# Performance work log

Hardware: AMD Instinct MI355X
Metric: run time of the kernel (lower is better)

## Reference

```python
import jax, jax.numpy as jnp
import numpy as np

B, S, HID = 2, 2048, 2048
NH, NKV, D = 32, 8, 64
G = NH // NKV
THETA = 150000.0


def rotate_half(x):
    x1, x2 = x[..., : D // 2], x[..., D // 2 :]
    return jnp.concatenate([-x2, x1], axis=-1)


def setup_inputs() -> dict:
    key = jax.random.key(0)
    ks = jax.random.split(key, 10)
    sc = 0.02
    return {
        "hidden_states": jax.random.normal(ks[0], (B, S, HID), jnp.float32),
        "position_ids": jnp.arange(S, dtype=jnp.int64 if jax.config.jax_enable_x64 else jnp.int32),
        "wq": jax.random.normal(ks[1], (HID, NH * D), jnp.float32) * sc,
        "bq": jax.random.normal(ks[2], (NH * D,), jnp.float32) * sc,
        "wk": jax.random.normal(ks[3], (HID, NKV * D), jnp.float32) * sc,
        "bk": jax.random.normal(ks[4], (NKV * D,), jnp.float32) * sc,
        "wv": jax.random.normal(ks[5], (HID, NKV * D), jnp.float32) * sc,
        "bv": jax.random.normal(ks[6], (NKV * D,), jnp.float32) * sc,
        "wo": jax.random.normal(ks[7], (NH * D, HID), jnp.float32) * sc,
        "bo": jax.random.normal(ks[8], (HID,), jnp.float32) * sc,
    }


def reference(hidden_states, position_ids, wq, bq, wk, bk, wv, bv, wo, bo):
    # projections: [B,S,NH,D] / [B,S,NKV,D] -> head-major
    q = (hidden_states @ wq + bq).reshape(B, S, NH, D).transpose(0, 2, 1, 3)   # [B,NH,S,D]
    k = (hidden_states @ wk + bk).reshape(B, S, NKV, D).transpose(0, 2, 1, 3)  # [B,NKV,S,D]
    v = (hidden_states @ wv + bv).reshape(B, S, NKV, D).transpose(0, 2, 1, 3)

    # HF RoPE: inv_freq over even dims, freqs duplicated across the two halves
    inv_freq = 1.0 / (THETA ** (jnp.arange(0, D, 2, dtype=jnp.float32) / D))   # [D/2]
    freqs = position_ids.astype(jnp.float32)[:, None] * inv_freq[None, :]      # [S,D/2]
    emb = jnp.concatenate([freqs, freqs], axis=-1)                             # [S,D]
    cos = jnp.cos(emb)[None, None]  # [1,1,S,D]
    sin = jnp.sin(emb)[None, None]
    q = q * cos + rotate_half(q) * sin
    k = k * cos + rotate_half(k) * sin

    # GQA: group query heads by kv head instead of repeat_interleave on K/V
    qg = q.reshape(B, NKV, G, S, D)
    scores = jnp.einsum("bkgsd,bktd->bkgst", qg, k) / jnp.sqrt(jnp.float32(D))  # [B,NKV,G,S,S]
    attn = jax.nn.softmax(scores, axis=-1)
    out = jnp.einsum("bkgst,bktd->bkgsd", attn, v)                              # [B,NKV,G,S,D]
    out = out.reshape(B, NH, S, D).transpose(0, 2, 1, 3).reshape(B, S, NH * D)  # [B,S,NH*D]
    return out @ wo + bo
```

## Files before the change

### kernel.cpp

```cpp
#include <hip/hip_runtime.h>
#include <hip/hip_bf16.h>
#include <math.h>

#define B_   2
#define S_   2048
#define HID_ 2048
#define NH_  32
#define NKV_ 8
#define D_   64
#define G_   (NH_/NKV_)
#define M_   (B_*S_)

typedef __hip_bfloat16 bf16;
typedef short bf16x8 __attribute__((ext_vector_type(8)));
typedef float f32x4  __attribute__((ext_vector_type(4)));
typedef unsigned short u16x4 __attribute__((ext_vector_type(4)));

__device__ inline unsigned short f2bfu(float f){
    __hip_bfloat16 h = __float2bfloat16(f);
    return __builtin_bit_cast(unsigned short, h);
}

__device__ __forceinline__ float fexp2(float x){
#if __has_builtin(__builtin_amdgcn_exp2f)
    return __builtin_amdgcn_exp2f(x);
#else
    return exp2f(x);
#endif
}

__device__ __forceinline__ void async16(const void* g, void* l) {
    __builtin_amdgcn_global_load_lds(
        (const __attribute__((address_space(1))) unsigned int*)g,
        (__attribute__((address_space(3))) unsigned int*)l, 16, 0, 0);
}

__global__ __launch_bounds__(256) void cvt_k(
    const float* __restrict__ src, bf16* __restrict__ dst, int n)
{
    const int i = (blockIdx.x * 256 + threadIdx.x) * 8;
    if (i >= n) return;
    const float4 a = *(const float4*)(src + i);
    const float4 b = *(const float4*)(src + i + 4);
    uint4 u;
    u.x = (unsigned)f2bfu(a.x) | ((unsigned)f2bfu(a.y) << 16);
    u.y = (unsigned)f2bfu(a.z) | ((unsigned)f2bfu(a.w) << 16);
    u.z = (unsigned)f2bfu(b.x) | ((unsigned)f2bfu(b.y) << 16);
    u.w = (unsigned)f2bfu(b.z) | ((unsigned)f2bfu(b.w) << 16);
    *(uint4*)((unsigned short*)dst + i) = u;
}

__global__ __launch_bounds__(256) void wtrans_k(
    const float* __restrict__ s0, int N0,
    const float* __restrict__ s1, int N1,
    const float* __restrict__ s2, int N2,
    bf16* __restrict__ dst, int K)
{
    __shared__ unsigned short t[64][65];
    const int ntile = blockIdx.x * 64, ktile = blockIdx.y * 64;
    const float* src; int nloc, Nseg;
    if (ntile < N0)           { src = s0; nloc = ntile;           Nseg = N0; }
    else if (ntile < N0 + N1) { src = s1; nloc = ntile - N0;      Nseg = N1; }
    else                      { src = s2; nloc = ntile - N0 - N1; Nseg = N2; }
    const int r  = threadIdx.x >> 4;
    const int c4 = (threadIdx.x & 15) * 4;
    #pragma unroll
    for (int p = 0; p < 4; p++) {
        const int k = p * 16 + r;
        const float4 f = *(const float4*)(src + (size_t)(ktile + k) * Nseg + nloc + c4);
        t[k][c4+0] = f2bfu(f.x); t[k][c4+1] = f2bfu(f.y);
        t[k][c4+2] = f2bfu(f.z); t[k][c4+3] = f2bfu(f.w);
    }
    __syncthreads();
    #pragma unroll
    for (int p = 0; p < 4; p++) {
        const int n = p * 16 + r;
        u16x4 u = { t[c4+0][n], t[c4+1][n], t[c4+2][n], t[c4+3][n] };
        *(u16x4*)((unsigned short*)dst + (size_t)(ntile + n) * K + ktile + c4) = u;
    }
}

__global__ __launch_bounds__(256) void rope_tab_k(
    const int* __restrict__ pos, float* __restrict__ ctab, float* __restrict__ stab)
{
    const int idx = blockIdx.x * 256 + threadIdx.x;
    if (idx >= S_ * 32) return;
    const int s = idx >> 5, i = idx & 31;
    const int is64 = (pos[1] == 0);
    const int p = is64 ? pos[2 * s] : pos[s];
    const double inv = exp(-(double)i * (log(150000.0) / 32.0));
    const double f = (double)p * inv;
    ctab[idx] = (float)cos(f);
    stab[idx] = (float)sin(f);
}

template<int MODE>
__global__ __launch_bounds__(256) void gemm128_k(
    const bf16* __restrict__ A, const bf16* __restrict__ WT,
    const float* __restrict__ b0, const float* __restrict__ b1,
    const float* __restrict__ b2,
    bf16* __restrict__ Cq, bf16* __restrict__ Ck, bf16* __restrict__ Cv,
    float* __restrict__ Cout,
    const float* __restrict__ ctab, const float* __restrict__ stab)
{
    __shared__ unsigned short sA[128 * 64];
    __shared__ unsigned short sB[128 * 64];

    const int tid  = threadIdx.x;
    const int wave = tid >> 6, lane = tid & 63;
    const int li   = lane & 15, lj = lane >> 4;
    const int m0   = blockIdx.y * 128;
    const int n0   = blockIdx.x * 128;
    const int wm   = (wave >> 1) * 64, wn = (wave & 1) * 64;
    const int K    = 2048;

    f32x4 acc[4][4];
    #pragma unroll
    for (int i = 0; i < 4; i++)
        #pragma unroll
        for (int j = 0; j < 4; j++)
            acc[i][j] = (f32x4){0.f, 0.f, 0.f, 0.f};

    const bf16* ag = A  + (size_t)(m0 + wave * 32 + (lane >> 3)) * K + (lane & 7) * 8;
    const bf16* bg = WT + (size_t)(n0 + wave * 32 + (lane >> 3)) * K + (lane & 7) * 8;
    unsigned short* la = &sA[(wave * 32) * 64];
    unsigned short* lb = &sB[(wave * 32) * 64];

    for (int k0 = 0; k0 < K; k0 += 64) {
        __syncthreads();
        #pragma unroll
        for (int i = 0; i < 4; i++) {
            async16(ag + k0 + (size_t)i * 8 * K, la + i * 8 * 64);
            async16(bg + k0 + (size_t)i * 8 * K, lb + i * 8 * 64);
        }
        __syncthreads();

        #pragma unroll
        for (int ks = 0; ks < 64; ks += 32) {
            bf16x8 af[4], bfr[4];
            #pragma unroll
            for (int mt = 0; mt < 4; mt++)
                af[mt] = *(const bf16x8*)&sA[(wm + mt * 16 + li) * 64 + ks + lj * 8];
            #pragma unroll
            for (int nt = 0; nt < 4; nt++)
                bfr[nt] = *(const bf16x8*)&sB[(wn + nt * 16 + li) * 64 + ks + lj * 8];
            #pragma unroll
            for (int mt = 0; mt < 4; mt++)
                #pragma unroll
                for (int nt = 0; nt < 4; nt++)
                    acc[mt][nt] = __builtin_amdgcn_mfma_f32_16x16x32_bf16(
                        af[mt], bfr[nt], acc[mt][nt], 0, 0, 0);
        }
    }

    if (MODE == 1) {
        #pragma unroll
        for (int mt = 0; mt < 4; mt++)
            #pragma unroll
            for (int nt = 0; nt < 4; nt++) {
                const int col = n0 + wn + nt * 16 + li;
                const float bb = b0[col];
                #pragma unroll
                for (int r = 0; r < 4; r++) {
                    const int row = m0 + wm + mt * 16 + lj * 4 + r;
                    Cout[(size_t)row * HID_ + col] = acc[mt][nt][r] + bb;
                }
            }
        return;
    }

    int seg, cb; const float* bias;
    if (n0 < 2048)      { seg = 0; cb = n0;        bias = b0; }
    else if (n0 < 2560) { seg = 1; cb = n0 - 2048; bias = b1; }
    else                { seg = 2; cb = n0 - 2560; bias = b2; }

    float bl[4];
    #pragma unroll
    for (int nt = 0; nt < 4; nt++) bl[nt] = bias[cb + wn + nt * 16 + li];

    if (seg == 2) {
        const int b = m0 >> 11;
        #pragma unroll
        for (int nt = 0; nt < 4; nt++) {
            const int cseg = cb + wn + nt * 16 + li;
            const int hv = cseg >> 6, d = cseg & 63;
            #pragma unroll
            for (int mt = 0; mt < 4; mt++) {
                const int sb = (m0 & (S_ - 1)) + wm + mt * 16 + lj * 4;
                u16x4 u = { f2bfu(acc[mt][nt][0] + bl[nt]),
                            f2bfu(acc[mt][nt][1] + bl[nt]),
                            f2bfu(acc[mt][nt][2] + bl[nt]),
                            f2bfu(acc[mt][nt][3] + bl[nt]) };
                *(u16x4*)((unsigned short*)Cv +
                    ((size_t)((b * NKV_ + hv) * 64 + d)) * S_ + sb) = u;
            }
        }
        return;
    }

    const float qs = (seg == 0) ? 0.18033688011112042f : 1.0f;
    #pragma unroll
    for (int mt = 0; mt < 4; mt++) {
        #pragma unroll
        for (int r = 0; r < 4; r++) {
            const int row = m0 + wm + mt * 16 + lj * 4 + r;
            const int s = row & (S_ - 1);
            const float c0  = ctab[s * 32 + li],      sn0 = stab[s * 32 + li];
            const float c1  = ctab[s * 32 + 16 + li], sn1 = stab[s * 32 + 16 + li];
            const float x0 = acc[mt][0][r] + bl[0];
            const float x1 = acc[mt][1][r] + bl[1];
            const float x2 = acc[mt][2][r] + bl[2];
            const float x3 = acc[mt][3][r] + bl[3];
            const float y0 = (x0 * c0 - x2 * sn0) * qs;
            const float y2 = (x2 * c0 + x0 * sn0) * qs;
            const float y1 = (x1 * c1 - x3 * sn1) * qs;
            const float y3 = (x3 * c1 + x1 * sn1) * qs;
            if (seg == 0) {
                bf16* cp = Cq + (size_t)row * HID_ + n0 + wn + li;
                cp[0]  = __float2bfloat16(y0);
                cp[16] = __float2bfloat16(y1);
                cp[32] = __float2bfloat16(y2);
                cp[48] = __float2bfloat16(y3);
            } else {
                bf16* cp = Ck + (size_t)row * 512 + cb + wn + li;
                cp[0]  = __float2bfloat16(y0);
                cp[16] = __float2bfloat16(y1);
                cp[32] = __float2bfloat16(y2);
                cp[48] = __float2bfloat16(y3);
            }
        }
    }
}

__global__ __launch_bounds__(256) void attn_k(
    const bf16* __restrict__ qws, const bf16* __restrict__ kws,
    const bf16* __restrict__ vtw, bf16* __restrict__ ows)
{
    __shared__ unsigned short sK [64][72];
    __shared__ unsigned short sVt[64][72];
    __shared__ unsigned short sP [4][16][72];

    const int tid  = threadIdx.x;
    const int wave = tid >> 6, lane = tid & 63;
    const int li   = lane & 15, lj = lane >> 4;
    const int bh   = blockIdx.y;
    const int q0   = blockIdx.x * 64;
    const int b    = bh / NH_, h = bh % NH_;
    const int hk   = h / G_;

    bf16x8 qf[2];
    {
        const bf16* qp = qws + (size_t)(b * S_ + q0 + wave * 16 + li) * HID_
                         + h * D_ + lj * 8;
        qf[0] = *(const bf16x8*)(qp);
        qf[1] = *(const bf16x8*)(qp + 32);
    }

    f32x4 o[4];
    #pragma unroll
    for (int mt = 0; mt < 4; mt++) o[mt] = (f32x4){0.f, 0.f, 0.f, 0.f};
    float mr = -1e30f, ll = 0.f;

    const int srow = tid >> 2, scol = (tid & 3) * 16;
    const bf16* kb = kws + (size_t)b * S_ * 512 + hk * 64;
    const bf16* vb = vtw + (size_t)((b * NKV_ + hk) * 64) * S_;

    for (int kt = 0; kt < S_; kt += 64) {
        const uint4* kp = (const uint4*)(kb + (size_t)(kt + srow) * 512 + scol);
        const uint4* vp = (const uint4*)(vb + (size_t)srow * S_ + kt + scol);
        const uint4 k0 = kp[0], k1 = kp[1];
        const uint4 v0 = vp[0], v1 = vp[1];

        __syncthreads();
        *(uint4*)&sK [srow][scol]     = k0;
        *(uint4*)&sK [srow][scol + 8] = k1;
        *(uint4*)&sVt[srow][scol]     = v0;
        *(uint4*)&sVt[srow][scol + 8] = v1;
        __syncthreads();

        float sc[4][4];
        #pragma unroll
        for (int nt = 0; nt < 4; nt++) {
            f32x4 c = (f32x4){0.f, 0.f, 0.f, 0.f};
            #pragma unroll
            for (int ks = 0; ks < 2; ks++) {
                const bf16x8 kf = *(const bf16x8*)&sK[nt * 16 + li][ks * 32 + lj * 8];
                c = __builtin_amdgcn_mfma_f32_16x16x32_bf16(kf, qf[ks], c, 0, 0, 0);
            }
            #pragma unroll
            for (int r = 0; r < 4; r++) sc[nt][r] = c[r];
        }

        float cm = sc[0][0];
        #pragma unroll
        for (int nt = 0; nt < 4; nt++)
            #pragma unroll
            for (int r = 0; r < 4; r++) cm = fmaxf(cm, sc[nt][r]);
        cm = fmaxf(cm, __shfl_xor(cm, 16));
        cm = fmaxf(cm, __shfl_xor(cm, 32));
        const float mnew  = fmaxf(mr, cm);
        const float alpha = fexp2(mr - mnew);
        mr = mnew;
        float rs = 0.f;
        #pragma unroll
        for (int nt = 0; nt < 4; nt++)
            #pragma unroll
            for (int r = 0; r < 4; r++) {
                sc[nt][r] = fexp2(sc[nt][r] - mnew);
                rs += sc[nt][r];
            }
        rs += __shfl_xor(rs, 16);
        rs += __shfl_xor(rs, 32);
        ll = ll * alpha + rs;
        #pragma unroll
        for (int mt = 0; mt < 4; mt++) o[mt] *= alpha;

        #pragma unroll
        for (int nt = 0; nt < 4; nt++) {
            u16x4 u = { f2bfu(sc[nt][0]), f2bfu(sc[nt][1]),
                        f2bfu(sc[nt][2]), f2bfu(sc[nt][3]) };
            *(u16x4*)&sP[wave][li][nt * 16 + lj * 4] = u;
        }

        #pragma unroll
        for (int ks = 0; ks < 2; ks++) {
            const bf16x8 pf = *(const bf16x8*)&sP[wave][li][ks * 32 + lj * 8];
            #pragma unroll
            for (int mt = 0; mt < 4; mt++) {
                const bf16x8 vf = *(const bf16x8*)&sVt[mt * 16 + li][ks * 32 + lj * 8];
                o[mt] = __builtin_amdgcn_mfma_f32_16x16x32_bf16(vf, pf, o[mt], 0, 0, 0);
            }
        }
    }

    const float inv = 1.0f / ll;
    bf16* op = ows + (size_t)(b * S_ + q0 + wave * 16 + li) * HID_ + h * D_;
    #pragma unroll
    for (int mt = 0; mt < 4; mt++) {
        u16x4 u = { f2bfu(o[mt][0] * inv), f2bfu(o[mt][1] * inv),
                    f2bfu(o[mt][2] * inv), f2bfu(o[mt][3] * inv) };
        *(u16x4*)((unsigned short*)op + mt * 16 + lj * 4) = u;
    }
}

extern "C" void kernel_launch(void* const* d_in, const int* in_sizes, int n_in,
                              void* d_out, int out_size, void* d_ws, size_t ws_size,
                              hipStream_t stream)
{
    const float* hs  = (const float*)d_in[0];
    const int*   pos = (const int*)d_in[1];
    const float* wq = (const float*)d_in[2];
    const float* bq = (const float*)d_in[3];
    const float* wk = (const float*)d_in[4];
    const float* bk = (const float*)d_in[5];
    const float* wv = (const float*)d_in[6];
    const float* bv = (const float*)d_in[7];
    const float* wo = (const float*)d_in[8];
    const float* bo = (const float*)d_in[9];

    char* ws = (char*)d_ws;
    float* ctab  = (float*)(ws);
    float* stab  = (float*)(ws + (256u << 10));
    bf16*  k_ws  = (bf16*)(ws + (512u << 10));
    bf16*  v_t   = (bf16*)(ws + (512u << 10) + (4u  << 20));
    bf16*  q_ws  = (bf16*)(ws + (512u << 10) + (8u  << 20));
    bf16*  woT   = q_ws;
    bf16*  hs_b  = (bf16*)(ws + (512u << 10) + (24u << 20));
    bf16*  o_ws  = hs_b;
    bf16*  wqkvT = (bf16*)(ws + (512u << 10) + (40u << 20));

    rope_tab_k<<<dim3(256), dim3(256), 0, stream>>>(pos, ctab, stab);

    cvt_k<<<dim3(M_ * HID_ / 2048), dim3(256), 0, stream>>>(hs, hs_b, M_ * HID_);

    wtrans_k<<<dim3(48, 32), dim3(256), 0, stream>>>(
        wq, 2048, wk, 512, wv, 512, wqkvT, HID_);

    gemm128_k<0><<<dim3(24, 32), dim3(256), 0, stream>>>(
        hs_b, wqkvT, bq, bk, bv, q_ws, k_ws, v_t, nullptr, ctab, stab);

    attn_k<<<dim3(S_ / 64, B_ * NH_), dim3(256), 0, stream>>>(q_ws, k_ws, v_t, o_ws);

    wtrans_k<<<dim3(32, 32), dim3(256), 0, stream>>>(
        wo, 2048, wo, 0, wo, 0, woT, HID_);

    gemm128_k<1><<<dim3(16, 32), dim3(256), 0, stream>>>(
        o_ws, woT, bo, nullptr, nullptr, nullptr, nullptr, nullptr,
        (float*)d_out, nullptr, nullptr);
}
```

Measured before the change: 399.5 us.

## Double query rows per wave in attention, swizzle LDS, prefetch K/V, lazy rescale

The attention kernel now handles 128 query rows per block, 32 per wave, so each K/V fragment read from LDS feeds two MFMA groups. It drops padded LDS arrays in favour of an XOR swizzle and prefetches the next K/V tile into registers while the current one is computed. Online-softmax rescaling is skipped unless the running max grows by more than a threshold, and row sums are now reduced across lanes only once at the end. It also adds setprio hints around the MFMA phases and a launch-bounds occupancy hint. The cost is more registers per wave and half as many blocks in the grid.

```diff
diff --git a/kernel.cpp b/kernel.cpp
--- a/kernel.cpp
+++ b/kernel.cpp
@@ -34,6 +34,8 @@
         (const __attribute__((address_space(1))) unsigned int*)g,
         (__attribute__((address_space(3))) unsigned int*)l, 16, 0, 0);
 }
+
+#define SWZ(r, c) ((c) ^ (((r) & 7) << 3))
 
 __global__ __launch_bounds__(256) void cvt_k(
     const float* __restrict__ src, bf16* __restrict__ dst, int n)
@@ -232,114 +234,143 @@
     }
 }
 
-__global__ __launch_bounds__(256) void attn_k(
+__global__ __launch_bounds__(256, 4) void attn_k(
     const bf16* __restrict__ qws, const bf16* __restrict__ kws,
     const bf16* __restrict__ vtw, bf16* __restrict__ ows)
 {
-    __shared__ unsigned short sK [64][72];
-    __shared__ unsigned short sVt[64][72];
-    __shared__ unsigned short sP [4][16][72];
+    __shared__ unsigned short sK [64 * 64];
+    __shared__ unsigned short sVt[64 * 64];
+    __shared__ unsigned short sP [4 * 32 * 64];
 
     const int tid  = threadIdx.x;
     const int wave = tid >> 6, lane = tid & 63;
     const int li   = lane & 15, lj = lane >> 4;
     const int bh   = blockIdx.y;
-    const int q0   = blockIdx.x * 64;
+    const int q0   = blockIdx.x * 128;
     const int b    = bh / NH_, h = bh % NH_;
     const int hk   = h / G_;
 
-    bf16x8 qf[2];
-    {
-        const bf16* qp = qws + (size_t)(b * S_ + q0 + wave * 16 + li) * HID_
+    bf16x8 qf[2][2];
+    #pragma unroll
+    for (int g = 0; g < 2; g++) {
+        const bf16* qp = qws + (size_t)(b * S_ + q0 + wave * 32 + g * 16 + li) * HID_
                          + h * D_ + lj * 8;
-        qf[0] = *(const bf16x8*)(qp);
-        qf[1] = *(const bf16x8*)(qp + 32);
-    }
-
-    f32x4 o[4];
-    #pragma unroll
-    for (int mt = 0; mt < 4; mt++) o[mt] = (f32x4){0.f, 0.f, 0.f, 0.f};
-    float mr = -1e30f, ll = 0.f;
+        qf[g][0] = *(const bf16x8*)(qp);
+        qf[g][1] = *(const bf16x8*)(qp + 32);
+    }
+
+    f32x4 o[2][4];
+    #pragma unroll
+    for (int g = 0; g < 2; g++)
+        #pragma unroll
+        for (int mt = 0; mt < 4; mt++) o[g][mt] = (f32x4){0.f, 0.f, 0.f, 0.f};
+    float mr[2] = {-1e30f, -1e30f};
+    float ll[2] = {0.f, 0.f};
 
     const int srow = tid >> 2, scol = (tid & 3) * 16;
     const bf16* kb = kws + (size_t)b * S_ * 512 + hk * 64;
     const bf16* vb = vtw + (size_t)((b * NKV_ + hk) * 64) * S_;
+    unsigned short* sp = sP + wave * (32 * 64);
+
+    uint4 pk0, pk1, pv0, pv1;
+    {
+        const uint4* kp = (const uint4*)(kb + (size_t)srow * 512 + scol);
+        const uint4* vp = (const uint4*)(vb + (size_t)srow * S_ + scol);
+        pk0 = kp[0]; pk1 = kp[1]; pv0 = vp[0]; pv1 = vp[1];
+    }
 
     for (int kt = 0; kt < S_; kt += 64) {
-        const uint4* kp = (const uint4*)(kb + (size_t)(kt + srow) * 512 + scol);
-        const uint4* vp = (const uint4*)(vb + (size_t)srow * S_ + kt + scol);
-        const uint4 k0 = kp[0], k1 = kp[1];
-        const uint4 v0 = vp[0], v1 = vp[1];
-
         __syncthreads();
-        *(uint4*)&sK [srow][scol]     = k0;
-        *(uint4*)&sK [srow][scol + 8] = k1;
-        *(uint4*)&sVt[srow][scol]     = v0;
-        *(uint4*)&sVt[srow][scol + 8] = v1;
+        *(uint4*)&sK [srow * 64 + SWZ(srow, scol)]     = pk0;
+        *(uint4*)&sK [srow * 64 + SWZ(srow, scol + 8)] = pk1;
+        *(uint4*)&sVt[srow * 64 + SWZ(srow, scol)]     = pv0;
+        *(uint4*)&sVt[srow * 64 + SWZ(srow, scol + 8)] = pv1;
         __syncthreads();
 
-        float sc[4][4];
+        if (kt + 64 < S_) {
+            const uint4* kp = (const uint4*)(kb + (size_t)(kt + 64 + srow) * 512 + scol);
+            const uint4* vp = (const uint4*)(vb + (size_t)srow * S_ + kt + 64 + scol);
+            pk0 = kp[0]; pk1 = kp[1]; pv0 = vp[0]; pv1 = vp[1];
+        }
+
+        float sc[2][4][4];
+        __builtin_amdgcn_s_setprio(1);
         #pragma unroll
         for (int nt = 0; nt < 4; nt++) {
-            f32x4 c = (f32x4){0.f, 0.f, 0.f, 0.f};
+            f32x4 c0 = (f32x4){0.f, 0.f, 0.f, 0.f};
+            f32x4 c1 = (f32x4){0.f, 0.f, 0.f, 0.f};
             #pragma unroll
             for (int ks = 0; ks < 2; ks++) {
-                const bf16x8 kf = *(const bf16x8*)&sK[nt * 16 + li][ks * 32 + lj * 8];
-                c = __builtin_amdgcn_mfma_f32_16x16x32_bf16(kf, qf[ks], c, 0, 0, 0);
-            }
-            #pragma unroll
-            for (int r = 0; r < 4; r++) sc[nt][r] = c[r];
-        }
-
-        float cm = sc[0][0];
-        #pragma unroll
-        for (int nt = 0; nt < 4; nt++)
-            #pragma unroll
-            for (int r = 0; r < 4; r++) cm = fmaxf(cm, sc[nt][r]);
-        cm = fmaxf(cm, __shfl_xor(cm, 16));
-        cm = fmaxf(cm, __shfl_xor(cm, 32));
-        const float mnew  = fmaxf(mr, cm);
-        const float alpha = fexp2(mr - mnew);
-        mr = mnew;
-        float rs = 0.f;
-        #pragma unroll
-        for (int nt = 0; nt < 4; nt++)
-            #pragma unroll
-            for (int r = 0; r < 4; r++) {
-                sc[nt][r] = fexp2(sc[nt][r] - mnew);
-                rs += sc[nt][r];
-            }
-        rs += __shfl_xor(rs, 16);
-        rs += __shfl_xor(rs, 32);
-        ll = ll * alpha + rs;
-        #pragma unroll
-        for (int mt = 0; mt < 4; mt++) o[mt] *= alpha;
-
-        #pragma unroll
-        for (int nt = 0; nt < 4; nt++) {
-            u16x4 u = { f2bfu(sc[nt][0]), f2bfu(sc[nt][1]),
-                        f2bfu(sc[nt][2]), f2bfu(sc[nt][3]) };
-            *(u16x4*)&sP[wave][li][nt * 16 + lj * 4] = u;
-        }
-
+                const bf16x8 kf =
+                    *(const bf16x8*)&sK[(nt * 16 + li) * 64 + SWZ(li, ks * 32 + lj * 8)];
+                c0 = __builtin_amdgcn_mfma_f32_16x16x32_bf16(kf, qf[0][ks], c0, 0, 0, 0);
+                c1 = __builtin_amdgcn_mfma_f32_16x16x32_bf16(kf, qf[1][ks], c1, 0, 0, 0);
+            }
+            #pragma unroll
+            for (int r = 0; r < 4; r++) { sc[0][nt][r] = c0[r]; sc[1][nt][r] = c1[r]; }
+        }
+        __builtin_amdgcn_s_setprio(0);
+
+        #pragma unroll
+        for (int g = 0; g < 2; g++) {
+            float cm = sc[g][0][0];
+            #pragma unroll
+            for (int nt = 0; nt < 4; nt++)
+                #pragma unroll
+                for (int r = 0; r < 4; r++) cm = fmaxf(cm, sc[g][nt][r]);
+            cm = fmaxf(cm, __shfl_xor(cm, 16));
+            cm = fmaxf(cm, __shfl_xor(cm, 32));
+            if (!__all(cm - mr[g] <= 8.0f)) {
+                const float mnew = fmaxf(mr[g], cm);
+                const float al   = fexp2(mr[g] - mnew);
+                mr[g] = mnew;
+                ll[g] *= al;
+                #pragma unroll
+                for (int mt = 0; mt < 4; mt++) o[g][mt] *= al;
+            }
+            float rs = 0.f;
+            #pragma unroll
+            for (int nt = 0; nt < 4; nt++) {
+                const float e0 = fexp2(sc[g][nt][0] - mr[g]);
+                const float e1 = fexp2(sc[g][nt][1] - mr[g]);
+                const float e2 = fexp2(sc[g][nt][2] - mr[g]);
+                const float e3 = fexp2(sc[g][nt][3] - mr[g]);
+                rs += (e0 + e1) + (e2 + e3);
+                u16x4 u = { f2bfu(e0), f2bfu(e1), f2bfu(e2), f2bfu(e3) };
+                *(u16x4*)&sp[(g * 16 + li) * 64 + SWZ(li, nt * 16 + lj * 4)] = u;
+            }
+            ll[g] += rs;
+        }
+
+        __builtin_amdgcn_s_setprio(1);
         #pragma unroll
         for (int ks = 0; ks < 2; ks++) {
-            const bf16x8 pf = *(const bf16x8*)&sP[wave][li][ks * 32 + lj * 8];
+            const bf16x8 pf0 = *(const bf16x8*)&sp[(li)      * 64 + SWZ(li, ks * 32 + lj * 8)];
+            const bf16x8 pf1 = *(const bf16x8*)&sp[(16 + li) * 64 + SWZ(li, ks * 32 + lj * 8)];
             #pragma unroll
             for (int mt = 0; mt < 4; mt++) {
-                const bf16x8 vf = *(const bf16x8*)&sVt[mt * 16 + li][ks * 32 + lj * 8];
-                o[mt] = __builtin_amdgcn_mfma_f32_16x16x32_bf16(vf, pf, o[mt], 0, 0, 0);
-            }
-        }
-    }
-
-    const float inv = 1.0f / ll;
-    bf16* op = ows + (size_t)(b * S_ + q0 + wave * 16 + li) * HID_ + h * D_;
-    #pragma unroll
-    for (int mt = 0; mt < 4; mt++) {
-        u16x4 u = { f2bfu(o[mt][0] * inv), f2bfu(o[mt][1] * inv),
-                    f2bfu(o[mt][2] * inv), f2bfu(o[mt][3] * inv) };
-        *(u16x4*)((unsigned short*)op + mt * 16 + lj * 4) = u;
+                const bf16x8 vf =
+                    *(const bf16x8*)&sVt[(mt * 16 + li) * 64 + SWZ(li, ks * 32 + lj * 8)];
+                o[0][mt] = __builtin_amdgcn_mfma_f32_16x16x32_bf16(vf, pf0, o[0][mt], 0, 0, 0);
+                o[1][mt] = __builtin_amdgcn_mfma_f32_16x16x32_bf16(vf, pf1, o[1][mt], 0, 0, 0);
+            }
+        }
+        __builtin_amdgcn_s_setprio(0);
+    }
+
+    #pragma unroll
+    for (int g = 0; g < 2; g++) {
+        float l = ll[g];
+        l += __shfl_xor(l, 16);
+        l += __shfl_xor(l, 32);
+        const float inv = 1.0f / l;
+        bf16* op = ows + (size_t)(b * S_ + q0 + wave * 32 + g * 16 + li) * HID_ + h * D_;
+        #pragma unroll
+        for (int mt = 0; mt < 4; mt++) {
+            u16x4 u = { f2bfu(o[g][mt][0] * inv), f2bfu(o[g][mt][1] * inv),
+                        f2bfu(o[g][mt][2] * inv), f2bfu(o[g][mt][3] * inv) };
+            *(u16x4*)((unsigned short*)op + mt * 16 + lj * 4) = u;
+        }
     }
 }
 
@@ -379,7 +410,7 @@
     gemm128_k<0><<<dim3(24, 32), dim3(256), 0, stream>>>(
         hs_b, wqkvT, bq, bk, bv, q_ws, k_ws, v_t, nullptr, ctab, stab);
 
-    attn_k<<<dim3(S_ / 64, B_ * NH_), dim3(256), 0, stream>>>(q_ws, k_ws, v_t, o_ws);
+    attn_k<<<dim3(S_ / 128, B_ * NH_), dim3(256), 0, stream>>>(q_ws, k_ws, v_t, o_ws);
 
     wtrans_k<<<dim3(32, 32), dim3(256), 0, stream>>>(
         wo, 2048, wo, 0, wo, 0, woT, HID_);
```

Measured after the change: 371.4 us. -7.0%, faster.
